# Kernel tuning notes

Hardware: AMD Instinct MI355X
Metric: run time of the kernel (lower is better)

The kernel has to match this reference:

```python
import jax, jax.numpy as jnp
import numpy as np

D_MODEL = 1024
N_HEADS = 16


def setup_inputs() -> dict:
    key = jax.random.key(0)
    ks = jax.random.split(key, 10)
    d = D_MODEL
    # xavier-uniform-ish linear weights
    lim = float(np.sqrt(6.0 / (d + d)))
    def lin_w(k):
        return jax.random.uniform(k, (d, d), jnp.float32, -lim, lim)
    inp = {
        "x": jax.random.normal(ks[0], (1, 2048, d), jnp.float32),
        "Wq": lin_w(ks[1]), "bq": jnp.zeros((d,), jnp.float32),
        "Wk": lin_w(ks[2]), "bk": jnp.zeros((d,), jnp.float32),
        "Wv": lin_w(ks[3]), "bv": jnp.zeros((d,), jnp.float32),
        "Wo": lin_w(ks[4]), "bo": jnp.zeros((d,), jnp.float32),
        "beta": 0.1 * jax.random.normal(ks[5], (N_HEADS,), jnp.float32),
        "n_heads": N_HEADS,
    }
    return inp


def reference(x, Wq, bq, Wk, bk, Wv, bv, Wo, bo, beta, n_heads):
    B, S, D = x.shape
    H = n_heads
    dh = D // H
    # projections, split heads: b s (h d) -> b h s d
    def proj(W, b):
        y = jnp.einsum('bsD,dD->bsd', x, W) + b
        return y.reshape(B, S, H, dh).transpose(0, 2, 1, 3)
    q = proj(Wq, bq)
    k = proj(Wk, bk)
    v = proj(Wv, bv)
    # per-head scale: sqrt(d_head) * exp(beta)
    scale = (jnp.sqrt(jnp.asarray(dh, x.dtype)) * jnp.exp(beta))[None, :, None, None]
    q = jax.nn.softplus(q / scale)
    k = jax.nn.softplus(k / scale)
    # causal linear attention: cumulative k (x) v outer products  [b h s d e]
    kv = jnp.cumsum(k[..., :, None] * v[..., None, :], axis=2)
    k1 = jnp.cumsum(k, axis=2)
    num = jnp.einsum('bhsd,bhsde->bhse', q, kv)
    den = jnp.sum(q * k1, axis=-1, keepdims=True)
    out = num / den
    out = out.transpose(0, 2, 1, 3).reshape(B, S, D)
    return jnp.einsum('bsD,dD->bsd', out, Wo) + bo
```

## Files before the change

kernel.cpp:

```cpp
#include <hip/hip_runtime.h>
#include <hip/hip_bf16.h>
#include <math.h>

#define S_LEN 2048
#define DM    1024
#define NH    16
#define DH    64
#define CHUNK 64
#define NCH   (S_LEN / CHUNK)
#define ST_STRIDE (DH * DH + DH)

typedef __attribute__((ext_vector_type(8))) short bf16x8;
typedef __attribute__((ext_vector_type(4))) float f32x4;

__device__ __forceinline__ float softplus_f(float x) {
    return (x > 20.0f) ? x : __logf(1.0f + __expf(x));
}

__device__ __forceinline__ ushort bf16r(float f) {
    union { float f; unsigned int u; } c; c.f = f;
    unsigned int u = c.u;
    u = (u + 0x7FFFu + ((u >> 16) & 1u)) >> 16;
    return (ushort)u;
}

__device__ __forceinline__ float b2f(ushort u) {
    union { unsigned int i; float f; } c; c.i = ((unsigned int)u) << 16;
    return c.f;
}

__global__ __launch_bounds__(256)
void cast_all_kernel(const float* __restrict__ x,
                     const float* __restrict__ Wq, const float* __restrict__ Wk,
                     const float* __restrict__ Wv, const float* __restrict__ Wo,
                     ushort* __restrict__ x_bf, ushort* __restrict__ w_bf)
{
    const int y = blockIdx.y;
    const float* src;
    ushort* dst;
    if (y < 2) { src = x + (size_t)y * (DM * DM);  dst = x_bf + (size_t)y * (DM * DM); }
    else {
        const float* ws[4] = {Wq, Wk, Wv, Wo};
        src = ws[y - 2];  dst = w_bf + (size_t)(y - 2) * (DM * DM);
    }
    const int i = (blockIdx.x * 256 + threadIdx.x) * 4;
    const float4 v = *(const float4*)(src + i);
    ushort4 o; o.x = bf16r(v.x); o.y = bf16r(v.y); o.z = bf16r(v.z); o.w = bf16r(v.w);
    *(ushort4*)(dst + i) = o;
}

__global__ __launch_bounds__(256)
void qkv_gemm_kernel(const ushort* __restrict__ Xb, const ushort* __restrict__ Wqkv,
                     const float* __restrict__ bq, const float* __restrict__ bk,
                     const float* __restrict__ bv,
                     const float* __restrict__ beta,
                     ushort* __restrict__ qkv )
{
    __shared__ ushort Als[64 * 128];
    __shared__ ushort Bls[128 * 128];

    const int b = blockIdx.x;
    const int logical = (b & 7) * 96 + (b >> 3);
    const int mb = logical & 31, nb = logical >> 5;
    const int m0 = mb * 64, n0 = nb * 128;
    const int z  = nb >> 3;
    const int nz0 = (nb & 7) * 128;
    const float* bias = (z == 0) ? bq : (z == 1) ? bk : bv;

    const int t = threadIdx.x, w = t >> 6, l = t & 63;
    const int wr = w >> 1, wc = w & 1;
    const int rsub = l >> 4;
    const int frow = l & 15, kq = l >> 4;

    f32x4 acc[2][4];
#pragma unroll
    for (int mi = 0; mi < 2; ++mi)
#pragma unroll
        for (int ni = 0; ni < 4; ++ni) acc[mi][ni] = (f32x4){0.f, 0.f, 0.f, 0.f};

    for (int kt = 0; kt < DM; kt += 128) {
#pragma unroll
        for (int k2 = 0; k2 < 12; ++k2) {
            const int idx = w + 4 * k2;
            const int r8g = ((idx & 1) << 2) | rsub;
            const int scol = (((l & 15) ^ r8g) << 3);
            if (idx < 16) {
                __builtin_amdgcn_global_load_lds(
                    (const __attribute__((address_space(1))) void*)(Xb + (size_t)(m0 + idx * 4 + rsub) * DM + kt + scol),
                    (__attribute__((address_space(3))) void*)(Als + idx * 512), 16, 0, 0);
            } else {
                const int ib = idx - 16;
                __builtin_amdgcn_global_load_lds(
                    (const __attribute__((address_space(1))) void*)(Wqkv + (size_t)(n0 + ib * 4 + rsub) * DM + kt + scol),
                    (__attribute__((address_space(3))) void*)(Bls + ib * 512), 16, 0, 0);
            }
        }
        __syncthreads();

#pragma unroll
        for (int ks = 0; ks < 4; ++ks) {
            bf16x8 af[2], bf[4];
#pragma unroll
            for (int mi = 0; mi < 2; ++mi) {
                const int rr = wr * 32 + mi * 16 + frow;
                af[mi] = *(const bf16x8*)&Als[rr * 128 + (((ks * 4 + kq) ^ (rr & 7)) << 3)];
            }
#pragma unroll
            for (int ni = 0; ni < 4; ++ni) {
                const int rr = wc * 64 + ni * 16 + frow;
                bf[ni] = *(const bf16x8*)&Bls[rr * 128 + (((ks * 4 + kq) ^ (rr & 7)) << 3)];
            }
#pragma unroll
            for (int mi = 0; mi < 2; ++mi)
#pragma unroll
                for (int ni = 0; ni < 4; ++ni)
                    acc[mi][ni] = __builtin_amdgcn_mfma_f32_16x16x32_bf16(af[mi], bf[ni], acc[mi][ni], 0, 0, 0);
        }
        __syncthreads();
    }

    ushort* outz = qkv + (size_t)z * (NH * S_LEN * DH);
    const int hwave = (nz0 >> 6) + wc;
    const float inv = (z < 2) ? (1.0f / (8.0f * __expf(beta[hwave]))) : 1.0f;
#pragma unroll
    for (int ni = 0; ni < 4; ++ni) {
        const int col = nz0 + wc * 64 + ni * 16 + (l & 15);
        const int d = col & 63;
        const float bcol = bias[col];
#pragma unroll
        for (int mi = 0; mi < 2; ++mi) {
            const int rbase = m0 + wr * 32 + mi * 16 + (l >> 4) * 4;
#pragma unroll
            for (int r = 0; r < 4; ++r) {
                float v = acc[mi][ni][r] + bcol;
                if (z < 2) v = softplus_f(v * inv);
                outz[((size_t)hwave * S_LEN + rbase + r) * DH + d] = bf16r(v);
            }
        }
    }
}

__global__ __launch_bounds__(256)
void o_gemm_kernel(const ushort* __restrict__ Ab, const ushort* __restrict__ Wob,
                   const float* __restrict__ bo, float* __restrict__ out)
{
    __shared__ ushort Als[64 * 128];
    __shared__ ushort Bls[64 * 128];

    const int b = blockIdx.x;
    const int logical = (b & 7) * 64 + (b >> 3);
    const int mb = logical & 31, nb = logical >> 5;
    const int m0 = mb * 64, n0 = nb * 64;

    const int t = threadIdx.x, w = t >> 6, l = t & 63;
    const int wr = w >> 1, wc = w & 1;
    const int rsub = l >> 4;
    const int frow = l & 15, kq = l >> 4;

    f32x4 acc[2][2];
#pragma unroll
    for (int mi = 0; mi < 2; ++mi)
#pragma unroll
        for (int ni = 0; ni < 2; ++ni) acc[mi][ni] = (f32x4){0.f, 0.f, 0.f, 0.f};

    for (int kt = 0; kt < DM; kt += 128) {
#pragma unroll
        for (int k2 = 0; k2 < 8; ++k2) {
            const int idx = w + 4 * k2;
            const int r8g = ((idx & 1) << 2) | rsub;
            const int scol = (((l & 15) ^ r8g) << 3);
            if (idx < 16) {
                __builtin_amdgcn_global_load_lds(
                    (const __attribute__((address_space(1))) void*)(Ab + (size_t)(m0 + idx * 4 + rsub) * DM + kt + scol),
                    (__attribute__((address_space(3))) void*)(Als + idx * 512), 16, 0, 0);
            } else {
                const int ib = idx - 16;
                __builtin_amdgcn_global_load_lds(
                    (const __attribute__((address_space(1))) void*)(Wob + (size_t)(n0 + ib * 4 + rsub) * DM + kt + scol),
                    (__attribute__((address_space(3))) void*)(Bls + ib * 512), 16, 0, 0);
            }
        }
        __syncthreads();

#pragma unroll
        for (int ks = 0; ks < 4; ++ks) {
            bf16x8 af[2], bf[2];
#pragma unroll
            for (int mi = 0; mi < 2; ++mi) {
                const int rr = wr * 32 + mi * 16 + frow;
                af[mi] = *(const bf16x8*)&Als[rr * 128 + (((ks * 4 + kq) ^ (rr & 7)) << 3)];
            }
#pragma unroll
            for (int ni = 0; ni < 2; ++ni) {
                const int rr = wc * 32 + ni * 16 + frow;
                bf[ni] = *(const bf16x8*)&Bls[rr * 128 + (((ks * 4 + kq) ^ (rr & 7)) << 3)];
            }
#pragma unroll
            for (int mi = 0; mi < 2; ++mi)
#pragma unroll
                for (int ni = 0; ni < 2; ++ni)
                    acc[mi][ni] = __builtin_amdgcn_mfma_f32_16x16x32_bf16(af[mi], bf[ni], acc[mi][ni], 0, 0, 0);
        }
        __syncthreads();
    }

#pragma unroll
    for (int ni = 0; ni < 2; ++ni) {
        const int col = n0 + wc * 32 + ni * 16 + (l & 15);
        const float bcol = bo[col];
#pragma unroll
        for (int mi = 0; mi < 2; ++mi) {
            const int rbase = m0 + wr * 32 + mi * 16 + (l >> 4) * 4;
#pragma unroll
            for (int r = 0; r < 4; ++r)
                out[(size_t)(rbase + r) * DM + col] = acc[mi][ni][r] + bcol;
        }
    }
}

__global__ __launch_bounds__(256)
void chunk_state_kernel(const ushort* __restrict__ k_ws, const ushort* __restrict__ v_ws,
                        float* __restrict__ st)
{
    __shared__ float Ks[64 * 64];
    __shared__ float Vs[64 * 64];
    const int c = blockIdx.x, h = blockIdx.y;
    const int t = threadIdx.x;
    const ushort* Kg = k_ws + ((size_t)h * S_LEN + c * CHUNK) * DH;
    const ushort* Vg = v_ws + ((size_t)h * S_LEN + c * CHUNK) * DH;
#pragma unroll
    for (int u = 0; u < 4; ++u) {
        int f = u * 256 + t;
        const ushort4 k4 = ((const ushort4*)Kg)[f];
        const ushort4 v4 = ((const ushort4*)Vg)[f];
        float* kp = Ks + f * 4;
        float* vp = Vs + f * 4;
        kp[0] = b2f(k4.x); kp[1] = b2f(k4.y); kp[2] = b2f(k4.z); kp[3] = b2f(k4.w);
        vp[0] = b2f(v4.x); vp[1] = b2f(v4.y); vp[2] = b2f(v4.z); vp[3] = b2f(v4.w);
    }
    __syncthreads();

    const int tx = t & 15, ty = t >> 4;
    float acc[4][4];
#pragma unroll
    for (int i = 0; i < 4; ++i)
#pragma unroll
        for (int j = 0; j < 4; ++j) acc[i][j] = 0.0f;

    for (int s = 0; s < 64; ++s) {
        const float4 ve = *(const float4*)&Vs[s * 64 + ty * 4];
        const float4 kd = *(const float4*)&Ks[s * 64 + tx * 4];
        const float vv[4] = {ve.x, ve.y, ve.z, ve.w};
        const float kv[4] = {kd.x, kd.y, kd.z, kd.w};
#pragma unroll
        for (int i = 0; i < 4; ++i)
#pragma unroll
            for (int j = 0; j < 4; ++j) acc[i][j] += vv[i] * kv[j];
    }
    float* base = st + (size_t)(h * NCH + c) * ST_STRIDE;
#pragma unroll
    for (int i = 0; i < 4; ++i) {
        float4 o; o.x = acc[i][0]; o.y = acc[i][1]; o.z = acc[i][2]; o.w = acc[i][3];
        *(float4*)(base + (ty * 4 + i) * 64 + tx * 4) = o;
    }
    if (t < 64) {
        float s = 0.0f;
        for (int j = 0; j < 64; ++j) s += Ks[j * 64 + t];
        base[DH * DH + t] = s;
    }
}

__global__ __launch_bounds__(64)
void scan_kernel(float* __restrict__ st, ushort* __restrict__ pfxT)
{
    const int h = blockIdx.y;
    const int e = blockIdx.x * 64 + threadIdx.x;
    float* p = st + (size_t)h * NCH * ST_STRIDE + e;
    ushort* pt = pfxT + (size_t)h * NCH * ST_STRIDE + e;
    float acc = 0.0f;
    for (int c = 0; c < NCH; ++c) {
        const float v = p[(size_t)c * ST_STRIDE];
        p[(size_t)c * ST_STRIDE] = acc;
        pt[(size_t)c * ST_STRIDE] = bf16r(acc);
        acc += v;
    }
}

__global__ __launch_bounds__(256)
void attn_out_kernel(const ushort* __restrict__ q_ws, const ushort* __restrict__ k_ws,
                     const ushort* __restrict__ v_ws, const float* __restrict__ pfx,
                     const ushort* __restrict__ pfxT, ushort* __restrict__ out_pre)
{
    __shared__ ushort Vt[64 * 64];
    __shared__ ushort Ps[64 * 64];
    __shared__ float denA[64];
    __shared__ float rsA[64];

    const int c = blockIdx.x, h = blockIdx.y;
    const int t = threadIdx.x, w = t >> 6, l = t & 63;
    const int fr = l & 15, fg = l >> 4;
    const int iw0 = w * 16;
    const size_t cbase = ((size_t)h * S_LEN + c * CHUNK) * DH;
    const ushort* Qg = q_ws + cbase;
    const ushort* Kg = k_ws + cbase;
    const ushort* Vg = v_ws + cbase;
    const float*  pb = pfx  + (size_t)(h * NCH + c) * ST_STRIDE;
    const ushort* pT = pfxT + (size_t)(h * NCH + c) * ST_STRIDE;

    {
        const int s = t >> 2, e0 = (t & 3) * 16;
        ushort vv[16];
        *(ushort4*)(vv + 0)  = *(const ushort4*)(Vg + s * 64 + e0);
        *(ushort4*)(vv + 4)  = *(const ushort4*)(Vg + s * 64 + e0 + 4);
        *(ushort4*)(vv + 8)  = *(const ushort4*)(Vg + s * 64 + e0 + 8);
        *(ushort4*)(vv + 12) = *(const ushort4*)(Vg + s * 64 + e0 + 12);
#pragma unroll
        for (int ee = 0; ee < 16; ++ee) {
            const int e = e0 + ee;
            Vt[e * 64 + ((((s >> 3) ^ (e & 7)) << 3) | (s & 7))] = vv[ee];
        }
    }

    bf16x8 qf[2], kf0, kf1;
#pragma unroll
    for (int kh = 0; kh < 2; ++kh)
        qf[kh] = *(const bf16x8*)(Qg + (iw0 + fr) * 64 + kh * 32 + fg * 8);

    f32x4 sacc[4];
#pragma unroll
    for (int jn = 0; jn < 4; ++jn) sacc[jn] = (f32x4){0.f, 0.f, 0.f, 0.f};
#pragma unroll
    for (int jn = 0; jn < 4; ++jn) {
        kf0 = *(const bf16x8*)(Kg + (jn * 16 + fr) * 64 + fg * 8);
        kf1 = *(const bf16x8*)(Kg + (jn * 16 + fr) * 64 + 32 + fg * 8);
        sacc[jn] = __builtin_amdgcn_mfma_f32_16x16x32_bf16(qf[0], kf0, sacc[jn], 0, 0, 0);
        sacc[jn] = __builtin_amdgcn_mfma_f32_16x16x32_bf16(qf[1], kf1, sacc[jn], 0, 0, 0);
    }

    float pr0 = 0.f, pr1 = 0.f, pr2 = 0.f, pr3 = 0.f;
#pragma unroll
    for (int jn = 0; jn < 4; ++jn) {
        const int j = jn * 16 + fr;
        const int gj = (jn * 2 + (fr >> 3));
#pragma unroll
        for (int r = 0; r < 4; ++r) {
            const int i = iw0 + fg * 4 + r;
            const float v = (j <= i) ? sacc[jn][r] : 0.0f;
            if (r == 0) pr0 += v; else if (r == 1) pr1 += v;
            else if (r == 2) pr2 += v; else pr3 += v;
            Ps[i * 64 + (((gj ^ (i & 7)) << 3) | (fr & 7))] = bf16r(v);
        }
    }
#pragma unroll
    for (int d = 1; d < 16; d <<= 1) {
        pr0 += __shfl_xor(pr0, d, 64);
        pr1 += __shfl_xor(pr1, d, 64);
        pr2 += __shfl_xor(pr2, d, 64);
        pr3 += __shfl_xor(pr3, d, 64);
    }
    if (fr == 0)      rsA[iw0 + fg * 4 + 0] = pr0;
    else if (fr == 1) rsA[iw0 + fg * 4 + 1] = pr1;
    else if (fr == 2) rsA[iw0 + fg * 4 + 2] = pr2;
    else if (fr == 3) rsA[iw0 + fg * 4 + 3] = pr3;

    float den = 0.f;
#pragma unroll
    for (int kh = 0; kh < 2; ++kh)
#pragma unroll
        for (int jj = 0; jj < 8; ++jj)
            den += b2f((ushort)qf[kh][jj]) * pb[DH * DH + kh * 32 + fg * 8 + jj];
    den += __shfl_xor(den, 16, 64);
    den += __shfl_xor(den, 32, 64);
    if (l < 16) denA[iw0 + l] = den;

    __syncthreads();

    bf16x8 paf[2];
#pragma unroll
    for (int kh = 0; kh < 2; ++kh)
        paf[kh] = *(const bf16x8*)&Ps[(iw0 + fr) * 64 + ((((kh * 4 + fg) ^ (fr & 7))) << 3)];

    f32x4 oacc[4];
#pragma unroll
    for (int jn = 0; jn < 4; ++jn) oacc[jn] = (f32x4){0.f, 0.f, 0.f, 0.f};
#pragma unroll
    for (int jn = 0; jn < 4; ++jn) {
        const int er = jn * 16 + fr;
        const bf16x8 vt0 = *(const bf16x8*)&Vt[er * 64 + ((((0 + fg) ^ (fr & 7))) << 3)];
        const bf16x8 vt1 = *(const bf16x8*)&Vt[er * 64 + ((((4 + fg) ^ (fr & 7))) << 3)];
        const bf16x8 tf0 = *(const bf16x8*)(pT + er * 64 + fg * 8);
        const bf16x8 tf1 = *(const bf16x8*)(pT + er * 64 + 32 + fg * 8);
        oacc[jn] = __builtin_amdgcn_mfma_f32_16x16x32_bf16(paf[0], vt0, oacc[jn], 0, 0, 0);
        oacc[jn] = __builtin_amdgcn_mfma_f32_16x16x32_bf16(paf[1], vt1, oacc[jn], 0, 0, 0);
        oacc[jn] = __builtin_amdgcn_mfma_f32_16x16x32_bf16(qf[0], tf0, oacc[jn], 0, 0, 0);
        oacc[jn] = __builtin_amdgcn_mfma_f32_16x16x32_bf16(qf[1], tf1, oacc[jn], 0, 0, 0);
    }

#pragma unroll
    for (int r = 0; r < 4; ++r) {
        const int i = iw0 + fg * 4 + r;
        const float rcp = 1.0f / (denA[i] + rsA[i]);
        const size_t rowb = (size_t)(c * CHUNK + i) * DM + h * DH;
#pragma unroll
        for (int jn = 0; jn < 4; ++jn)
            out_pre[rowb + jn * 16 + fr] = bf16r(oacc[jn][r] * rcp);
    }
}

extern "C" void kernel_launch(void* const* d_in, const int* in_sizes, int n_in,
                              void* d_out, int out_size, void* d_ws, size_t ws_size,
                              hipStream_t stream)
{
    const float* x    = (const float*)d_in[0];
    const float* Wq   = (const float*)d_in[1];
    const float* bq   = (const float*)d_in[2];
    const float* Wk   = (const float*)d_in[3];
    const float* bk   = (const float*)d_in[4];
    const float* Wv   = (const float*)d_in[5];
    const float* bv   = (const float*)d_in[6];
    const float* Wo   = (const float*)d_in[7];
    const float* bo   = (const float*)d_in[8];
    const float* beta = (const float*)d_in[9];
    float* out = (float*)d_out;

    ushort* q_ws  = (ushort*)d_ws;
    ushort* k_ws  = q_ws + (size_t)NH * S_LEN * DH;
    ushort* v_ws  = k_ws + (size_t)NH * S_LEN * DH;
    float*  st    = (float*)(v_ws + (size_t)NH * S_LEN * DH);
    ushort* x_bf  = (ushort*)(st + (size_t)NH * NCH * ST_STRIDE);
    ushort* w_bf  = x_bf + (size_t)S_LEN * DM;
    ushort* op_bf = w_bf + (size_t)4 * DM * DM;
    ushort* pfxT  = op_bf + (size_t)S_LEN * DM;

    const ushort* wo_bf = w_bf + (size_t)3 * DM * DM;

    cast_all_kernel<<<dim3((DM * DM) / 1024, 6), 256, 0, stream>>>(x, Wq, Wk, Wv, Wo, x_bf, w_bf);

    qkv_gemm_kernel<<<768, 256, 0, stream>>>(x_bf, w_bf, bq, bk, bv, beta, q_ws);

    chunk_state_kernel<<<dim3(NCH, NH), 256, 0, stream>>>(k_ws, v_ws, st);
    scan_kernel<<<dim3(ST_STRIDE / 64, NH), 64, 0, stream>>>(st, pfxT);
    attn_out_kernel<<<dim3(NCH, NH), 256, 0, stream>>>(q_ws, k_ws, v_ws, st, pfxT, op_bf);

    o_gemm_kernel<<<512, 256, 0, stream>>>(op_bf, wo_bf, bo, out);
}
```

Measured before the change: 65.23 us.

## Double-buffer QKV GEMM LDS tiles with async prefetch two stages ahead

Splits the QKV projection GEMM K-loop into 64-wide tiles held in two LDS buffers, issuing global_load_lds for the next stage while computing on the current one and using explicit vmcnt waits and barriers instead of full __syncthreads. The aim is to hide global memory latency behind MFMA work. In exchange the loop has more iterations and barriers, and the swizzle pattern changes to suit the narrower 64-column rows.

```diff
diff --git a/kernel.cpp b/kernel.cpp
--- a/kernel.cpp
+++ b/kernel.cpp
@@ -56,8 +56,11 @@
                      const float* __restrict__ beta,
                      ushort* __restrict__ qkv )
 {
-    __shared__ ushort Als[64 * 128];
-    __shared__ ushort Bls[128 * 128];
+    constexpr int ASZ = 64 * 64;
+    constexpr int BSZ = 128 * 64;
+    constexpr int NT  = 16;
+    __shared__ ushort Als[2 * ASZ];
+    __shared__ ushort Bls[2 * BSZ];
 
     const int b = blockIdx.x;
     const int logical = (b & 7) * 96 + (b >> 3);
@@ -69,7 +72,8 @@
 
     const int t = threadIdx.x, w = t >> 6, l = t & 63;
     const int wr = w >> 1, wc = w & 1;
-    const int rsub = l >> 4;
+    const int r8 = l >> 3;
+    const int scol = ((l & 7) ^ r8) * 8;
     const int frow = l & 15, kq = l >> 4;
 
     f32x4 acc[2][4];
@@ -78,37 +82,47 @@
 #pragma unroll
         for (int ni = 0; ni < 4; ++ni) acc[mi][ni] = (f32x4){0.f, 0.f, 0.f, 0.f};
 
-    for (int kt = 0; kt < DM; kt += 128) {
-#pragma unroll
-        for (int k2 = 0; k2 < 12; ++k2) {
+    auto STAGE = [&](int buf, int kt) {
+#pragma unroll
+        for (int k2 = 0; k2 < 6; ++k2) {
             const int idx = w + 4 * k2;
-            const int r8g = ((idx & 1) << 2) | rsub;
-            const int scol = (((l & 15) ^ r8g) << 3);
-            if (idx < 16) {
+            if (idx < 8) {
                 __builtin_amdgcn_global_load_lds(
-                    (const __attribute__((address_space(1))) void*)(Xb + (size_t)(m0 + idx * 4 + rsub) * DM + kt + scol),
-                    (__attribute__((address_space(3))) void*)(Als + idx * 512), 16, 0, 0);
+                    (const __attribute__((address_space(1))) void*)(Xb + (size_t)(m0 + idx * 8 + r8) * DM + kt + scol),
+                    (__attribute__((address_space(3))) void*)(Als + buf * ASZ + idx * 512), 16, 0, 0);
             } else {
-                const int ib = idx - 16;
+                const int ib = idx - 8;
                 __builtin_amdgcn_global_load_lds(
-                    (const __attribute__((address_space(1))) void*)(Wqkv + (size_t)(n0 + ib * 4 + rsub) * DM + kt + scol),
-                    (__attribute__((address_space(3))) void*)(Bls + ib * 512), 16, 0, 0);
-            }
-        }
-        __syncthreads();
-
-#pragma unroll
-        for (int ks = 0; ks < 4; ++ks) {
+                    (const __attribute__((address_space(1))) void*)(Wqkv + (size_t)(n0 + ib * 8 + r8) * DM + kt + scol),
+                    (__attribute__((address_space(3))) void*)(Bls + buf * BSZ + ib * 512), 16, 0, 0);
+            }
+        }
+    };
+
+    STAGE(0, 0);
+    STAGE(1, 64);
+
+    for (int tt = 0; tt < NT; ++tt) {
+        if (tt + 1 < NT) asm volatile("s_waitcnt vmcnt(6)" ::: "memory");
+        else             asm volatile("s_waitcnt vmcnt(0)" ::: "memory");
+        __builtin_amdgcn_s_barrier();
+        asm volatile("" ::: "memory");
+
+        const int cur = tt & 1;
+        const ushort* Ab_ = Als + cur * ASZ;
+        const ushort* Bb_ = Bls + cur * BSZ;
+#pragma unroll
+        for (int ks = 0; ks < 2; ++ks) {
             bf16x8 af[2], bf[4];
 #pragma unroll
             for (int mi = 0; mi < 2; ++mi) {
                 const int rr = wr * 32 + mi * 16 + frow;
-                af[mi] = *(const bf16x8*)&Als[rr * 128 + (((ks * 4 + kq) ^ (rr & 7)) << 3)];
+                af[mi] = *(const bf16x8*)&Ab_[rr * 64 + (((kq + 4 * ks) ^ (rr & 7)) << 3)];
             }
 #pragma unroll
             for (int ni = 0; ni < 4; ++ni) {
                 const int rr = wc * 64 + ni * 16 + frow;
-                bf[ni] = *(const bf16x8*)&Bls[rr * 128 + (((ks * 4 + kq) ^ (rr & 7)) << 3)];
+                bf[ni] = *(const bf16x8*)&Bb_[rr * 64 + (((kq + 4 * ks) ^ (rr & 7)) << 3)];
             }
 #pragma unroll
             for (int mi = 0; mi < 2; ++mi)
@@ -116,7 +130,11 @@
                 for (int ni = 0; ni < 4; ++ni)
                     acc[mi][ni] = __builtin_amdgcn_mfma_f32_16x16x32_bf16(af[mi], bf[ni], acc[mi][ni], 0, 0, 0);
         }
-        __syncthreads();
+
+        asm volatile("" ::: "memory");
+        __builtin_amdgcn_s_barrier();
+        asm volatile("" ::: "memory");
+        if (tt + 2 < NT) STAGE(cur, (tt + 2) * 64);
     }
 
     ushort* outz = qkv + (size_t)z * (NH * S_LEN * DH);
```

Result: no change. 64.20 us (-1.6%).
